# Optimization experiments

Hardware: AMD Instinct MI355X
Metric: run time of the kernel (lower is better)

Reference implementation:

```python
import jax, jax.numpy as jnp
import numpy as np

NUM_TOKENS = 2048
HIDDEN = 1024
INTER = 2048
NUM_EXPERTS = 8
TOPK = 2


def setup_inputs() -> dict:
    key = jax.random.key(0)
    k1, k2, k3, k4 = jax.random.split(key, 4)
    hidden_states = jax.random.normal(k1, (NUM_TOKENS, HIDDEN), dtype=jnp.float32)
    router_logits = jax.random.normal(k2, (NUM_TOKENS, NUM_EXPERTS), dtype=jnp.float32)
    # fc1: [E, hidden, 2*intermediate] (proj/gate for SwiGLU), fc2: [E, intermediate, hidden]
    w1 = jax.random.normal(k3, (NUM_EXPERTS, HIDDEN, 2 * INTER), dtype=jnp.float32) * 0.02
    w2 = jax.random.normal(k4, (NUM_EXPERTS, INTER, HIDDEN), dtype=jnp.float32) * 0.02
    return {"hidden_states": hidden_states, "router_logits": router_logits, "w1": w1, "w2": w2}


def _grouped_gemm(x, w, expert_ids):
    """x: [T, D], w: [E, D, O], expert_ids: [T] -> [T, O].
    Tokens are routed to expert expert_ids[t]; equivalent to the sequential
    per-expert GEMM on contiguously sorted tokens. Small fixed loop over E."""
    out = jnp.zeros((x.shape[0], w.shape[-1]), dtype=x.dtype)
    for e in range(w.shape[0]):
        mask = (expert_ids == e)[:, None]
        out = out + jnp.where(mask, x, 0.0) @ w[e]
    return out


def reference(hidden_states, router_logits, w1, w2):
    # top-k routing + softmax over the selected logits
    top_logits, top_idx = jax.lax.top_k(router_logits, TOPK)      # [N, K]
    scores = jax.nn.softmax(top_logits, axis=-1)                  # [N, K]

    flat_idx = top_idx.reshape(-1)                                # [N*K]
    sorted_indices = jnp.argsort(flat_idx)                        # permute tokens grouped by expert
    permuted = hidden_states[sorted_indices // TOPK]              # [N*K, D]
    sorted_experts = flat_idx[sorted_indices]                     # [N*K] expert id per permuted row

    fc1_out = _grouped_gemm(permuted, w1, sorted_experts)         # [N*K, 2*I]
    proj, gate = jnp.split(fc1_out, 2, axis=-1)
    act = jax.nn.silu(proj) * gate                                # SwiGLU
    expert_out = _grouped_gemm(act, w2, sorted_experts)           # [N*K, D]

    # unpermute (scatter back) and weighted combine over top-k
    unpermuted = jnp.zeros_like(expert_out).at[sorted_indices].set(expert_out)
    unpermuted = unpermuted.reshape(-1, TOPK, expert_out.shape[-1])
    return (unpermuted * scores[..., None]).sum(axis=1)           # [N, D]
```

## Files before the change

kernel.cpp:

```cpp
#include <hip/hip_runtime.h>
#include <hip/hip_bf16.h>

constexpr int T = 2048;
constexpr int H = 1024;
constexpr int I = 2048;
constexpr int N2 = 2 * I;
constexpr int RCAP = 5120;
constexpr int MAXT = 40;

constexpr int WS_OFF = 16;
constexpr int WS_TEXP = 32;
constexpr int WS_TOPKP = 4256;
constexpr int WS_ROWTOK = 8352;
constexpr int WS_TOKROW = 13472;
constexpr size_t WSB_ZROW = 114688;
constexpr size_t WSB_HSB  = 131072;
constexpr size_t WSB_ACT  = 8u << 20;
constexpr size_t WSB_PW1  = 32u << 20;
constexpr size_t WSB_PW2  = 96u << 20;

constexpr int W1T_BLKS = 8 * 32 * 8;
constexpr int W2T_BLKS = 8 * 64 * 2;
constexpr int HSB_BLKS = T * H / 2048;
constexpr int FC1_BLKS = 32 * MAXT;

typedef __attribute__((ext_vector_type(4))) float f32x4;
typedef __attribute__((ext_vector_type(8))) short s16x8;

__device__ __forceinline__ short f2bf(float f) {
    unsigned u = __float_as_uint(f);
    u += 0x7FFFu + ((u >> 16) & 1u);
    return (short)(u >> 16);
}

#define MFMA16(a, b, c) __builtin_amdgcn_mfma_f32_16x16x32_bf16(a, b, c, 0, 0, 0)

__device__ __forceinline__ void gl2lds16(const void* g, void* l) {
    __builtin_amdgcn_global_load_lds(
        (const __attribute__((address_space(1))) void*)g,
        (__attribute__((address_space(3))) void*)l, 16, 0, 0);
}

__global__ __launch_bounds__(256) void routing_hs_kernel(const float* __restrict__ logits,
                                                         int* __restrict__ wsi,
                                                         float* __restrict__ wsf,
                                                         const float* __restrict__ hs,
                                                         unsigned short* __restrict__ hsb) {
    const int t = threadIdx.x;
    if (blockIdx.x > 0) {
        int i = (((int)blockIdx.x - 1) * 256 + t) * 8;
        f32x4 a = *(const f32x4*)(hs + i);
        f32x4 b = *(const f32x4*)(hs + i + 4);
        s16x8 s = {f2bf(a[0]), f2bf(a[1]), f2bf(a[2]), f2bf(a[3]),
                   f2bf(b[0]), f2bf(b[1]), f2bf(b[2]), f2bf(b[3])};
        *(s16x8*)(hsb + i) = s;
        return;
    }
    __shared__ int cnt[8], base[9], fill[8];
    if (t < 8) { cnt[t] = 0; fill[t] = 0; }
    for (int r = t; r < RCAP; r += 256) wsi[WS_ROWTOK + r] = -1;
    unsigned short* zr = (unsigned short*)((char*)wsi + WSB_ZROW);
    for (int i = t; i < H; i += 256) zr[i] = 0;
    __syncthreads();

    int e0a[8], e1a[8];
    #pragma unroll
    for (int j = 0; j < 8; j++) {
        int tok = t * 8 + j;
        const float* l = logits + tok * 8;
        float v0 = -1e30f; int i0 = 0;
        #pragma unroll
        for (int i = 0; i < 8; i++) { float v = l[i]; if (v > v0) { v0 = v; i0 = i; } }
        float v1 = -1e30f; int i1 = 0;
        #pragma unroll
        for (int i = 0; i < 8; i++) { if (i == i0) continue; float v = l[i]; if (v > v1) { v1 = v; i1 = i; } }
        float ex = __expf(v1 - v0);
        float inv = 1.f / (1.f + ex);
        wsf[WS_TOPKP + tok * 2] = inv;
        wsf[WS_TOPKP + tok * 2 + 1] = ex * inv;
        e0a[j] = i0; e1a[j] = i1;
        atomicAdd(&cnt[i0], 1);
        atomicAdd(&cnt[i1], 1);
    }
    __syncthreads();
    if (t == 0) {
        int acc = 0;
        for (int e = 0; e < 8; e++) { base[e] = acc; acc += (cnt[e] + 127) & ~127; }
        base[8] = acc;
        for (int e = 0; e < 9; e++) wsi[WS_OFF + e] = base[e];
    }
    __syncthreads();
    for (int tt = t; tt < MAXT; tt += 256) {
        int rb = tt * 128, ex = 0;
        for (int e = 0; e < 8; e++)
            if (rb >= base[e] && rb < base[e + 1]) ex = e;
        wsi[WS_TEXP + tt] = ex;
    }
    #pragma unroll
    for (int j = 0; j < 8; j++) {
        int tok = t * 8 + j;
        int ee[2] = {e0a[j], e1a[j]};
        #pragma unroll
        for (int k = 0; k < 2; k++) {
            int e = ee[k];
            int slot = atomicAdd(&fill[e], 1);
            int r = base[e] + slot;
            wsi[WS_ROWTOK + r] = tok;
            wsi[WS_TOKROW + tok * 2 + k] = r;
        }
    }
}

__global__ __launch_bounds__(256) void prep_w1_kernel(
    const float* __restrict__ w1, unsigned short* __restrict__ pw1) {
    __shared__ __align__(16) unsigned short L[32 * 512];
    const int t = threadIdx.x;
    int b = blockIdx.x;
    int cs = b & 7, k0i = (b >> 3) & 31, e = b >> 8;
    const float* src = w1 + (size_t)e * H * N2 + (size_t)(k0i * 32) * N2 + cs * 512;
    #pragma unroll
    for (int i = 0; i < 8; i++) {
        int c = t + i * 256;
        int row = c >> 6, col8 = (c & 63) * 8;
        const float* sp = src + (size_t)row * N2 + col8;
        f32x4 a = *(const f32x4*)sp;
        f32x4 bb = *(const f32x4*)(sp + 4);
        s16x8 s = {f2bf(a[0]), f2bf(a[1]), f2bf(a[2]), f2bf(a[3]),
                   f2bf(bb[0]), f2bf(bb[1]), f2bf(bb[2]), f2bf(bb[3])};
        *(s16x8*)&L[c * 8] = s;
    }
    __syncthreads();
    int gate = cs >> 2;
    int ctbase = (cs & 3) * 8;
    unsigned short* dstb = pw1 + (size_t)(e * 1024 + k0i) * 4096;
    #pragma unroll
    for (int i = 0; i < 8; i++) {
        int cidx = t + i * 256;
        int within = cidx & 31, nhalf = (cidx >> 5) & 1;
        int kg = (cidx >> 6) & 3, ctp = cidx >> 8;
        int x = ctp * 64 + nhalf * 32 + within;
        int n = gate * 32 + nhalf * 64 + within;
        s16x8 s;
        #pragma unroll
        for (int kk = 0; kk < 8; kk++) s[kk] = (short)L[(kg * 8 + kk) * 512 + x];
        int ct = ctbase + ctp;
        *(s16x8*)(dstb + (size_t)ct * 32 * 4096 + (kg * 128 + n) * 8) = s;
    }
}

__global__ __launch_bounds__(256, 2) void fc1_kernel(
    const unsigned short* __restrict__ hsb, const unsigned short* __restrict__ pw1,
    const int* __restrict__ wsi, const unsigned short* __restrict__ zrow,
    unsigned short* __restrict__ act,
    const float* __restrict__ w2, unsigned short* __restrict__ pw2) {
    __shared__ __align__(16) unsigned short SM[32 * 512];
    const int t = threadIdx.x;

    if (blockIdx.x >= FC1_BLKS) {
        int b = (int)blockIdx.x - FC1_BLKS;
        int cs = b & 1, k0i = (b >> 1) & 63, e = b >> 7;
        const float* src = w2 + (size_t)e * I * H + (size_t)(k0i * 32) * H + cs * 512;
        #pragma unroll
        for (int i = 0; i < 8; i++) {
            int c = t + i * 256;
            int row = c >> 6, col8 = (c & 63) * 8;
            const float* sp = src + (size_t)row * H + col8;
            f32x4 a = *(const f32x4*)sp;
            f32x4 bb = *(const f32x4*)(sp + 4);
            s16x8 s = {f2bf(a[0]), f2bf(a[1]), f2bf(a[2]), f2bf(a[3]),
                       f2bf(bb[0]), f2bf(bb[1]), f2bf(bb[2]), f2bf(bb[3])};
            *(s16x8*)&SM[c * 8] = s;
        }
        __syncthreads();
        unsigned short* dstb = pw2 + (size_t)(e * 512 + k0i) * 4096;
        #pragma unroll
        for (int i = 0; i < 8; i++) {
            int cidx = t + i * 256;
            int n = cidx & 127, kg = (cidx >> 7) & 3, htp = cidx >> 9;
            int x = htp * 128 + n;
            s16x8 s;
            #pragma unroll
            for (int kk = 0; kk < 8; kk++) s[kk] = (short)SM[(kg * 8 + kk) * 512 + x];
            int ht = cs * 4 + htp;
            *(s16x8*)(dstb + (size_t)ht * 64 * 4096 + (kg * 128 + n) * 8) = s;
        }
        return;
    }

    unsigned short* Al = SM;
    unsigned short* Bl = SM + 4096;
    const int ct = blockIdx.x & 31, rt = blockIdx.x >> 5;
    const int rowb = rt * 128;
    if (rowb >= wsi[WS_OFF + 8]) return;
    const int e = wsi[WS_TEXP + rt];
    const unsigned short* pb = pw1 + (size_t)((e * 32 + ct) * 32) * 4096;

    const int m = t & 127;
    const int tok = wsi[WS_ROWTOK + rowb + m];
    const unsigned short* rp = (tok >= 0) ? (hsb + (size_t)tok * H) : zrow;
    const int kga = t >> 7;

    const int lane = t & 63, w = t >> 6, wr = w >> 1, wc = w & 1;
    const int q = lane >> 4, l16 = lane & 15;

    f32x4 zero = {0.f, 0.f, 0.f, 0.f};
    f32x4 acc[4][4];
    #pragma unroll
    for (int mi = 0; mi < 4; mi++)
        #pragma unroll
        for (int ni = 0; ni < 4; ni++) acc[mi][ni] = zero;

    for (int k0i = 0; k0i < 32; k0i++) {
        const int k0 = k0i * 32;
        gl2lds16(rp + k0 + kga * 8, &Al[t * 8]);
        gl2lds16(rp + k0 + (kga + 2) * 8, &Al[(t + 256) * 8]);
        const unsigned short* ps = pb + (size_t)k0i * 4096;
        gl2lds16(ps + t * 8, &Bl[t * 8]);
        gl2lds16(ps + (t + 256) * 8, &Bl[(t + 256) * 8]);
        __syncthreads();

        s16x8 af[4], bf[4];
        #pragma unroll
        for (int mi = 0; mi < 4; mi++)
            af[mi] = *(const s16x8*)&Al[(q * 128 + wr * 64 + mi * 16 + l16) * 8];
        #pragma unroll
        for (int ni = 0; ni < 4; ni++)
            bf[ni] = *(const s16x8*)&Bl[(q * 128 + wc * 64 + ni * 16 + l16) * 8];
        #pragma unroll
        for (int mi = 0; mi < 4; mi++)
            #pragma unroll
            for (int ni = 0; ni < 4; ni++)
                acc[mi][ni] = MFMA16(af[mi], bf[ni], acc[mi][ni]);
        __syncthreads();
    }

    #pragma unroll
    for (int mi = 0; mi < 4; mi++)
        #pragma unroll
        for (int r = 0; r < 4; r++) {
            int row = rowb + wr * 64 + mi * 16 + q * 4 + r;
            #pragma unroll
            for (int ni = 0; ni < 2; ni++) {
                int col = ct * 64 + wc * 32 + ni * 16 + l16;
                float p = acc[mi][ni][r], g = acc[mi][ni + 2][r];
                float val = p * g / (1.f + __expf(-p));
                act[(size_t)row * I + col] = (unsigned short)f2bf(val);
            }
        }
}

__global__ __launch_bounds__(256, 2) void fc2_kernel(
    const unsigned short* __restrict__ act, const unsigned short* __restrict__ pw2,
    const int* __restrict__ wsi, float* __restrict__ eo) {
    __shared__ __align__(16) unsigned short Al[512 * 8];
    __shared__ __align__(16) unsigned short Bl[512 * 8];
    const int t = threadIdx.x;
    const int ht = blockIdx.x, rt = blockIdx.y, ks = blockIdx.z;
    const int rowb = rt * 128;
    if (rowb >= wsi[WS_OFF + 8]) return;
    const int e = wsi[WS_TEXP + rt];
    const unsigned short* pb = pw2 + (size_t)((e * 8 + ht) * 64) * 4096;

    const int m = t & 127;
    const unsigned short* rp = act + (size_t)(rowb + m) * I;
    const int kga = t >> 7;

    const int lane = t & 63, w = t >> 6, wr = w >> 1, wc = w & 1;
    const int q = lane >> 4, l16 = lane & 15;

    f32x4 zero = {0.f, 0.f, 0.f, 0.f};
    f32x4 acc[4][4];
    #pragma unroll
    for (int mi = 0; mi < 4; mi++)
        #pragma unroll
        for (int ni = 0; ni < 4; ni++) acc[mi][ni] = zero;

    for (int k0i = ks * 32; k0i < ks * 32 + 32; k0i++) {
        const int k0 = k0i * 32;
        gl2lds16(rp + k0 + kga * 8, &Al[t * 8]);
        gl2lds16(rp + k0 + (kga + 2) * 8, &Al[(t + 256) * 8]);
        const unsigned short* ps = pb + (size_t)k0i * 4096;
        gl2lds16(ps + t * 8, &Bl[t * 8]);
        gl2lds16(ps + (t + 256) * 8, &Bl[(t + 256) * 8]);
        __syncthreads();

        s16x8 af[4], bf[4];
        #pragma unroll
        for (int mi = 0; mi < 4; mi++)
            af[mi] = *(const s16x8*)&Al[(q * 128 + wr * 64 + mi * 16 + l16) * 8];
        #pragma unroll
        for (int ni = 0; ni < 4; ni++)
            bf[ni] = *(const s16x8*)&Bl[(q * 128 + wc * 64 + ni * 16 + l16) * 8];
        #pragma unroll
        for (int mi = 0; mi < 4; mi++)
            #pragma unroll
            for (int ni = 0; ni < 4; ni++)
                acc[mi][ni] = MFMA16(af[mi], bf[ni], acc[mi][ni]);
        __syncthreads();
    }

    float* ed = eo + (size_t)ks * RCAP * H;
    #pragma unroll
    for (int mi = 0; mi < 4; mi++)
        #pragma unroll
        for (int r = 0; r < 4; r++) {
            int row = rowb + wr * 64 + mi * 16 + q * 4 + r;
            #pragma unroll
            for (int ni = 0; ni < 4; ni++) {
                int col = ht * 128 + wc * 64 + ni * 16 + l16;
                ed[(size_t)row * H + col] = acc[mi][ni][r];
            }
        }
}

__global__ __launch_bounds__(256) void combine_kernel(
    const float* __restrict__ eo, const int* __restrict__ wsi,
    const float* __restrict__ wsf, float* __restrict__ out) {
    const int tok = blockIdx.x;
    const int r0 = wsi[WS_TOKROW + tok * 2], r1 = wsi[WS_TOKROW + tok * 2 + 1];
    const float s0 = wsf[WS_TOPKP + tok * 2], s1 = wsf[WS_TOPKP + tok * 2 + 1];
    const float* a0 = eo + (size_t)r0 * H;
    const float* a1 = eo + (size_t)RCAP * H + (size_t)r0 * H;
    const float* b0 = eo + (size_t)r1 * H;
    const float* b1 = eo + (size_t)RCAP * H + (size_t)r1 * H;
    const int c = threadIdx.x * 4;
    f32x4 va0 = *(const f32x4*)(a0 + c), va1 = *(const f32x4*)(a1 + c);
    f32x4 vb0 = *(const f32x4*)(b0 + c), vb1 = *(const f32x4*)(b1 + c);
    f32x4 r;
    #pragma unroll
    for (int i = 0; i < 4; i++) r[i] = s0 * (va0[i] + va1[i]) + s1 * (vb0[i] + vb1[i]);
    *(f32x4*)(out + (size_t)tok * H + c) = r;
}

extern "C" void kernel_launch(void* const* d_in, const int* in_sizes, int n_in,
                              void* d_out, int out_size, void* d_ws, size_t ws_size,
                              hipStream_t stream) {
    const float* hs     = (const float*)d_in[0];
    const float* logits = (const float*)d_in[1];
    const float* w1     = (const float*)d_in[2];
    const float* w2     = (const float*)d_in[3];
    float* out = (float*)d_out;
    int* wsi = (int*)d_ws;
    float* wsf = (float*)d_ws;
    unsigned short* zrow = (unsigned short*)((char*)d_ws + WSB_ZROW);
    unsigned short* hsb  = (unsigned short*)((char*)d_ws + WSB_HSB);
    unsigned short* act  = (unsigned short*)((char*)d_ws + WSB_ACT);
    unsigned short* pw1  = (unsigned short*)((char*)d_ws + WSB_PW1);
    unsigned short* pw2  = (unsigned short*)((char*)d_ws + WSB_PW2);
    float* eo = (float*)((char*)d_ws + WSB_PW1);

    routing_hs_kernel<<<1 + HSB_BLKS, 256, 0, stream>>>(logits, wsi, wsf, hs, hsb);
    prep_w1_kernel<<<W1T_BLKS, 256, 0, stream>>>(w1, pw1);
    fc1_kernel<<<FC1_BLKS + W2T_BLKS, 256, 0, stream>>>(hsb, pw1, wsi, zrow, act, w2, pw2);
    fc2_kernel<<<dim3(8, MAXT, 2), 256, 0, stream>>>(act, pw2, wsi, eo);
    combine_kernel<<<T, 256, 0, stream>>>(eo, wsi, wsf, out);
}
```

Baseline: 372.1 us.

## Double-buffer LDS in fc1/fc2 GEMMs and merge w1 prep into routing kernel

The fc1 and fc2 main loops now use two LDS buffers, so the async global-to-LDS loads for the next K-slice are issued while MFMAs run on the current one. This halves the number of barriers per K step and hides load latency. The launch-bounds occupancy hint rises from 2 to 4 blocks per SM, which may pressure registers. The w1 repack kernel is folded into the routing/hs-conversion kernel to drop one launch and let those independent jobs run concurrently.

```diff
diff --git a/kernel.cpp b/kernel.cpp
--- a/kernel.cpp
+++ b/kernel.cpp
@@ -41,14 +41,52 @@
         (__attribute__((address_space(3))) void*)l, 16, 0, 0);
 }
 
-__global__ __launch_bounds__(256) void routing_hs_kernel(const float* __restrict__ logits,
-                                                         int* __restrict__ wsi,
-                                                         float* __restrict__ wsf,
-                                                         const float* __restrict__ hs,
-                                                         unsigned short* __restrict__ hsb) {
+__global__ __launch_bounds__(256) void pre_kernel(const float* __restrict__ logits,
+                                                  int* __restrict__ wsi,
+                                                  float* __restrict__ wsf,
+                                                  const float* __restrict__ hs,
+                                                  unsigned short* __restrict__ hsb,
+                                                  const float* __restrict__ w1,
+                                                  unsigned short* __restrict__ pw1) {
+    __shared__ __align__(16) unsigned short L[32 * 512];
     const int t = threadIdx.x;
-    if (blockIdx.x > 0) {
-        int i = (((int)blockIdx.x - 1) * 256 + t) * 8;
+
+    if (blockIdx.x < W1T_BLKS) {
+        int b = blockIdx.x;
+        int cs = b & 7, k0i = (b >> 3) & 31, e = b >> 8;
+        const float* src = w1 + (size_t)e * H * N2 + (size_t)(k0i * 32) * N2 + cs * 512;
+        #pragma unroll
+        for (int i = 0; i < 8; i++) {
+            int c = t + i * 256;
+            int row = c >> 6, col8 = (c & 63) * 8;
+            const float* sp = src + (size_t)row * N2 + col8;
+            f32x4 a = *(const f32x4*)sp;
+            f32x4 bb = *(const f32x4*)(sp + 4);
+            s16x8 s = {f2bf(a[0]), f2bf(a[1]), f2bf(a[2]), f2bf(a[3]),
+                       f2bf(bb[0]), f2bf(bb[1]), f2bf(bb[2]), f2bf(bb[3])};
+            *(s16x8*)&L[c * 8] = s;
+        }
+        __syncthreads();
+        int gate = cs >> 2;
+        int ctbase = (cs & 3) * 8;
+        unsigned short* dstb = pw1 + (size_t)(e * 1024 + k0i) * 4096;
+        #pragma unroll
+        for (int i = 0; i < 8; i++) {
+            int cidx = t + i * 256;
+            int within = cidx & 31, nhalf = (cidx >> 5) & 1;
+            int kg = (cidx >> 6) & 3, ctp = cidx >> 8;
+            int x = ctp * 64 + nhalf * 32 + within;
+            int n = gate * 32 + nhalf * 64 + within;
+            s16x8 s;
+            #pragma unroll
+            for (int kk = 0; kk < 8; kk++) s[kk] = (short)L[(kg * 8 + kk) * 512 + x];
+            int ct = ctbase + ctp;
+            *(s16x8*)(dstb + (size_t)ct * 32 * 4096 + (kg * 128 + n) * 8) = s;
+        }
+        return;
+    }
+    if (blockIdx.x > W1T_BLKS) {
+        int i = (((int)blockIdx.x - W1T_BLKS - 1) * 256 + t) * 8;
         f32x4 a = *(const f32x4*)(hs + i);
         f32x4 b = *(const f32x4*)(hs + i + 4);
         s16x8 s = {f2bf(a[0]), f2bf(a[1]), f2bf(a[2]), f2bf(a[3]),
@@ -56,7 +94,10 @@
         *(s16x8*)(hsb + i) = s;
         return;
     }
-    __shared__ int cnt[8], base[9], fill[8];
+
+    int* cnt  = (int*)L;
+    int* base = cnt + 8;
+    int* fill = base + 9;
     if (t < 8) { cnt[t] = 0; fill[t] = 0; }
     for (int r = t; r < RCAP; r += 256) wsi[WS_ROWTOK + r] = -1;
     unsigned short* zr = (unsigned short*)((char*)wsi + WSB_ZROW);
@@ -111,44 +152,7 @@
     }
 }
 
-__global__ __launch_bounds__(256) void prep_w1_kernel(
-    const float* __restrict__ w1, unsigned short* __restrict__ pw1) {
-    __shared__ __align__(16) unsigned short L[32 * 512];
-    const int t = threadIdx.x;
-    int b = blockIdx.x;
-    int cs = b & 7, k0i = (b >> 3) & 31, e = b >> 8;
-    const float* src = w1 + (size_t)e * H * N2 + (size_t)(k0i * 32) * N2 + cs * 512;
-    #pragma unroll
-    for (int i = 0; i < 8; i++) {
-        int c = t + i * 256;
-        int row = c >> 6, col8 = (c & 63) * 8;
-        const float* sp = src + (size_t)row * N2 + col8;
-        f32x4 a = *(const f32x4*)sp;
-        f32x4 bb = *(const f32x4*)(sp + 4);
-        s16x8 s = {f2bf(a[0]), f2bf(a[1]), f2bf(a[2]), f2bf(a[3]),
-                   f2bf(bb[0]), f2bf(bb[1]), f2bf(bb[2]), f2bf(bb[3])};
-        *(s16x8*)&L[c * 8] = s;
-    }
-    __syncthreads();
-    int gate = cs >> 2;
-    int ctbase = (cs & 3) * 8;
-    unsigned short* dstb = pw1 + (size_t)(e * 1024 + k0i) * 4096;
-    #pragma unroll
-    for (int i = 0; i < 8; i++) {
-        int cidx = t + i * 256;
-        int within = cidx & 31, nhalf = (cidx >> 5) & 1;
-        int kg = (cidx >> 6) & 3, ctp = cidx >> 8;
-        int x = ctp * 64 + nhalf * 32 + within;
-        int n = gate * 32 + nhalf * 64 + within;
-        s16x8 s;
-        #pragma unroll
-        for (int kk = 0; kk < 8; kk++) s[kk] = (short)L[(kg * 8 + kk) * 512 + x];
-        int ct = ctbase + ctp;
-        *(s16x8*)(dstb + (size_t)ct * 32 * 4096 + (kg * 128 + n) * 8) = s;
-    }
-}
-
-__global__ __launch_bounds__(256, 2) void fc1_kernel(
+__global__ __launch_bounds__(256, 4) void fc1_kernel(
     const unsigned short* __restrict__ hsb, const unsigned short* __restrict__ pw1,
     const int* __restrict__ wsi, const unsigned short* __restrict__ zrow,
     unsigned short* __restrict__ act,
@@ -187,8 +191,10 @@
         return;
     }
 
-    unsigned short* Al = SM;
-    unsigned short* Bl = SM + 4096;
+    unsigned short* A0 = SM;
+    unsigned short* B0 = SM + 4096;
+    unsigned short* A1 = SM + 8192;
+    unsigned short* B1 = SM + 12288;
     const int ct = blockIdx.x & 31, rt = blockIdx.x >> 5;
     const int rowb = rt * 128;
     if (rowb >= wsi[WS_OFF + 8]) return;
@@ -210,27 +216,40 @@
         #pragma unroll
         for (int ni = 0; ni < 4; ni++) acc[mi][ni] = zero;
 
-    for (int k0i = 0; k0i < 32; k0i++) {
-        const int k0 = k0i * 32;
-        gl2lds16(rp + k0 + kga * 8, &Al[t * 8]);
-        gl2lds16(rp + k0 + (kga + 2) * 8, &Al[(t + 256) * 8]);
-        const unsigned short* ps = pb + (size_t)k0i * 4096;
-        gl2lds16(ps + t * 8, &Bl[t * 8]);
-        gl2lds16(ps + (t + 256) * 8, &Bl[(t + 256) * 8]);
-        __syncthreads();
-
-        s16x8 af[4], bf[4];
-        #pragma unroll
-        for (int mi = 0; mi < 4; mi++)
-            af[mi] = *(const s16x8*)&Al[(q * 128 + wr * 64 + mi * 16 + l16) * 8];
-        #pragma unroll
-        for (int ni = 0; ni < 4; ni++)
-            bf[ni] = *(const s16x8*)&Bl[(q * 128 + wc * 64 + ni * 16 + l16) * 8];
-        #pragma unroll
-        for (int mi = 0; mi < 4; mi++)
-            #pragma unroll
-            for (int ni = 0; ni < 4; ni++)
-                acc[mi][ni] = MFMA16(af[mi], bf[ni], acc[mi][ni]);
+    #define FC1_STAGE(k0i, Ab, Bb)                                             \
+        do {                                                                   \
+            const int k0_ = (k0i) * 32;                                        \
+            gl2lds16(rp + k0_ + kga * 8, &(Ab)[t * 8]);                        \
+            gl2lds16(rp + k0_ + (kga + 2) * 8, &(Ab)[(t + 256) * 8]);          \
+            const unsigned short* ps_ = pb + (size_t)(k0i) * 4096;             \
+            gl2lds16(ps_ + t * 8, &(Bb)[t * 8]);                               \
+            gl2lds16(ps_ + (t + 256) * 8, &(Bb)[(t + 256) * 8]);               \
+        } while (0)
+
+    #define FC1_COMPUTE(Ab, Bb)                                                \
+        do {                                                                   \
+            s16x8 af[4], bf[4];                                                \
+            _Pragma("unroll")                                                  \
+            for (int mi = 0; mi < 4; mi++)                                     \
+                af[mi] = *(const s16x8*)&(Ab)[(q * 128 + wr * 64 + mi * 16 + l16) * 8]; \
+            _Pragma("unroll")                                                  \
+            for (int ni = 0; ni < 4; ni++)                                     \
+                bf[ni] = *(const s16x8*)&(Bb)[(q * 128 + wc * 64 + ni * 16 + l16) * 8]; \
+            _Pragma("unroll")                                                  \
+            for (int mi = 0; mi < 4; mi++)                                     \
+                _Pragma("unroll")                                              \
+                for (int ni = 0; ni < 4; ni++)                                 \
+                    acc[mi][ni] = MFMA16(af[mi], bf[ni], acc[mi][ni]);         \
+        } while (0)
+
+    FC1_STAGE(0, A0, B0);
+    __syncthreads();
+    for (int k0i = 0; k0i < 32; k0i += 2) {
+        FC1_STAGE(k0i + 1, A1, B1);
+        FC1_COMPUTE(A0, B0);
+        __syncthreads();
+        if (k0i + 2 < 32) FC1_STAGE(k0i + 2, A0, B0);
+        FC1_COMPUTE(A1, B1);
         __syncthreads();
     }
 
@@ -249,11 +268,14 @@
         }
 }
 
-__global__ __launch_bounds__(256, 2) void fc2_kernel(
+__global__ __launch_bounds__(256, 4) void fc2_kernel(
     const unsigned short* __restrict__ act, const unsigned short* __restrict__ pw2,
     const int* __restrict__ wsi, float* __restrict__ eo) {
-    __shared__ __align__(16) unsigned short Al[512 * 8];
-    __shared__ __align__(16) unsigned short Bl[512 * 8];
+    __shared__ __align__(16) unsigned short SM[32 * 512];
+    unsigned short* A0 = SM;
+    unsigned short* B0 = SM + 4096;
+    unsigned short* A1 = SM + 8192;
+    unsigned short* B1 = SM + 12288;
     const int t = threadIdx.x;
     const int ht = blockIdx.x, rt = blockIdx.y, ks = blockIdx.z;
     const int rowb = rt * 128;
@@ -275,27 +297,41 @@
         #pragma unroll
         for (int ni = 0; ni < 4; ni++) acc[mi][ni] = zero;
 
-    for (int k0i = ks * 32; k0i < ks * 32 + 32; k0i++) {
-        const int k0 = k0i * 32;
-        gl2lds16(rp + k0 + kga * 8, &Al[t * 8]);
-        gl2lds16(rp + k0 + (kga + 2) * 8, &Al[(t + 256) * 8]);
-        const unsigned short* ps = pb + (size_t)k0i * 4096;
-        gl2lds16(ps + t * 8, &Bl[t * 8]);
-        gl2lds16(ps + (t + 256) * 8, &Bl[(t + 256) * 8]);
-        __syncthreads();
-
-        s16x8 af[4], bf[4];
-        #pragma unroll
-        for (int mi = 0; mi < 4; mi++)
-            af[mi] = *(const s16x8*)&Al[(q * 128 + wr * 64 + mi * 16 + l16) * 8];
-        #pragma unroll
-        for (int ni = 0; ni < 4; ni++)
-            bf[ni] = *(const s16x8*)&Bl[(q * 128 + wc * 64 + ni * 16 + l16) * 8];
-        #pragma unroll
-        for (int mi = 0; mi < 4; mi++)
-            #pragma unroll
-            for (int ni = 0; ni < 4; ni++)
-                acc[mi][ni] = MFMA16(af[mi], bf[ni], acc[mi][ni]);
+    #define FC2_STAGE(k0i, Ab, Bb)                                             \
+        do {                                                                   \
+            const int k0_ = (k0i) * 32;                                        \
+            gl2lds16(rp + k0_ + kga * 8, &(Ab)[t * 8]);                        \
+            gl2lds16(rp + k0_ + (kga + 2) * 8, &(Ab)[(t + 256) * 8]);          \
+            const unsigned short* ps_ = pb + (size_t)(k0i) * 4096;             \
+            gl2lds16(ps_ + t * 8, &(Bb)[t * 8]);                               \
+            gl2lds16(ps_ + (t + 256) * 8, &(Bb)[(t + 256) * 8]);               \
+        } while (0)
+
+    #define FC2_COMPUTE(Ab, Bb)                                                \
+        do {                                                                   \
+            s16x8 af[4], bf[4];                                                \
+            _Pragma("unroll")                                                  \
+            for (int mi = 0; mi < 4; mi++)                                     \
+                af[mi] = *(const s16x8*)&(Ab)[(q * 128 + wr * 64 + mi * 16 + l16) * 8]; \
+            _Pragma("unroll")                                                  \
+            for (int ni = 0; ni < 4; ni++)                                     \
+                bf[ni] = *(const s16x8*)&(Bb)[(q * 128 + wc * 64 + ni * 16 + l16) * 8]; \
+            _Pragma("unroll")                                                  \
+            for (int mi = 0; mi < 4; mi++)                                     \
+                _Pragma("unroll")                                              \
+                for (int ni = 0; ni < 4; ni++)                                 \
+                    acc[mi][ni] = MFMA16(af[mi], bf[ni], acc[mi][ni]);         \
+        } while (0)
+
+    const int kb = ks * 32;
+    FC2_STAGE(kb, A0, B0);
+    __syncthreads();
+    for (int j = 0; j < 32; j += 2) {
+        FC2_STAGE(kb + j + 1, A1, B1);
+        FC2_COMPUTE(A0, B0);
+        __syncthreads();
+        if (j + 2 < 32) FC2_STAGE(kb + j + 2, A0, B0);
+        FC2_COMPUTE(A1, B1);
         __syncthreads();
     }
 
@@ -349,8 +385,7 @@
     unsigned short* pw2  = (unsigned short*)((char*)d_ws + WSB_PW2);
     float* eo = (float*)((char*)d_ws + WSB_PW1);
 
-    routing_hs_kernel<<<1 + HSB_BLKS, 256, 0, stream>>>(logits, wsi, wsf, hs, hsb);
-    prep_w1_kernel<<<W1T_BLKS, 256, 0, stream>>>(w1, pw1);
+    pre_kernel<<<W1T_BLKS + 1 + HSB_BLKS, 256, 0, stream>>>(logits, wsi, wsf, hs, hsb, w1, pw1);
     fc1_kernel<<<FC1_BLKS + W2T_BLKS, 256, 0, stream>>>(hsb, pw1, wsi, zrow, act, w2, pw2);
     fc2_kernel<<<dim3(8, MAXT, 2), 256, 0, stream>>>(act, pw2, wsi, eo);
     combine_kernel<<<T, 256, 0, stream>>>(eo, wsi, wsf, out);
```

Result: no change. 367.3 us (-1.3%).
